# Performance work log

Measured on AMD Instinct MI355X. Metric: run time of the kernel, lower is better.

The kernel has to match this reference:

```python
import jax, jax.numpy as jnp
import numpy as np

RADIUS_IN, RADIUS_OUT, NSAMPLE = 0.4, 0.8, 32
SCENE = 10.0  # cube edge length for point coordinates


def setup_inputs() -> dict:
    key = jax.random.key(0)
    k1, k2, k3 = jax.random.split(key, 3)
    B, N, NP, C = 2, 16384, 4096, 64
    xyz = jax.random.uniform(k1, (B, N, 3), dtype=jnp.float32) * SCENE
    new_xyz = jax.random.uniform(k2, (B, NP, 3), dtype=jnp.float32) * SCENE
    features = jax.random.normal(k3, (B, C, N), dtype=jnp.float32)
    return {"xyz": xyz, "new_xyz": new_xyz, "features": features}


def ball_query_dilated(xyz, new_xyz, min_r, max_r, nsample):
    # xyz: (B,N,3), new_xyz: (B,P,3) -> idx: (B,P,nsample) int32
    N = xyz.shape[1]
    d2 = jnp.sum((new_xyz[:, :, None, :] - xyz[:, None, :, :]) ** 2, axis=-1)  # (B,P,N)
    mask = (d2 >= min_r * min_r) & (d2 < max_r * max_r)
    ar = jnp.arange(N, dtype=jnp.int32)
    # valid points keep their index; invalid pushed after all valid ones, in order
    sort_key = jnp.where(mask, ar, ar + N)
    _, idx_sorted = jax.lax.top_k(-sort_key, nsample)  # first nsample in-range point indices
    cnt = jnp.sum(mask, axis=-1)  # (B,P)
    slot_valid = jnp.arange(nsample, dtype=cnt.dtype)[None, None, :] < cnt[:, :, None]
    # CUDA kernel fills all slots with the first found index; if none found idx stays 0
    # (when cnt==0, idx_sorted[...,0] == 0 since key N is the minimum), so this matches.
    idx = jnp.where(slot_valid, idx_sorted, idx_sorted[:, :, :1])
    return idx.astype(jnp.int32)


def group(features, idx):
    # features: (B,C,N), idx: (B,P,S) -> (B,C,P,S)
    return jax.vmap(lambda f, i: f[:, i])(features, idx)


def reference(xyz, new_xyz, features):
    idx = ball_query_dilated(xyz, new_xyz, RADIUS_IN, RADIUS_OUT, NSAMPLE)
    xyz_t = jnp.transpose(xyz, (0, 2, 1))  # (B,3,N)
    grouped_xyz = group(xyz_t, idx) - jnp.transpose(new_xyz, (0, 2, 1))[:, :, :, None]
    grouped_features = group(features, idx)
    new_features = jnp.concatenate([grouped_xyz, grouped_features], axis=1)  # (B,3+C,P,S)
    return new_features
```

## Files before the change

kernel.cpp:

```cpp
#include <hip/hip_runtime.h>
#include <hip/hip_bf16.h>

#define BB 2
#define NN 16384
#define NP 4096
#define CC 64
#define SS 32
#define NCH (3 + CC)

#define NSUB 32
#define SUBN (NN / NSUB)
#define QB 32

__global__ void __launch_bounds__(256) pack_xyz_kernel(
    const float* __restrict__ xyz, float4* __restrict__ xyz4)
{
    int i = blockIdx.x * 256 + threadIdx.x;
    if (i < BB * NN) {
        float4 v;
        v.x = xyz[3 * i + 0];
        v.y = xyz[3 * i + 1];
        v.z = xyz[3 * i + 2];
        v.w = 0.0f;
        xyz4[i] = v;
    }
}

__global__ void __launch_bounds__(256) transpose_feat_kernel(
    const float* __restrict__ f, float* __restrict__ ft)
{
    __shared__ float tile[64 * 65];
    const int b  = blockIdx.y;
    const int n0 = blockIdx.x * 64;
    const int t  = threadIdx.x;
    const int tn  = t & 63;
    const int tc4 = t >> 6;
#pragma unroll
    for (int r = 0; r < 16; ++r) {
        int c = r * 4 + tc4;
        tile[c * 65 + tn] = f[((b * CC + c) << 14) + n0 + tn];
    }
    __syncthreads();
#pragma unroll
    for (int r = 0; r < 16; ++r) {
        int nl = r * 4 + tc4;
        ft[((b << 14) + n0 + nl) * CC + tn] = tile[tn * 65 + nl];
    }
}

__global__ void __launch_bounds__(256) query_kernel(
    const float4* __restrict__ xyz4, const float* __restrict__ new_xyz,
    unsigned short* __restrict__ part, unsigned char* __restrict__ cntp)
{
#pragma clang fp contract(off)
    const int lane = threadIdx.x & 63;
    const int wid  = blockIdx.x * 4 + (threadIdx.x >> 6);
    const int b    = wid >> 12;
    const int r    = wid & 4095;
    const int sub  = r >> 7;
    const int qb   = r & 127;
    const int qbase = qb * QB;

    const float RMIN2 = (float)(0.4 * 0.4);
    const float RMAX2 = (float)(0.8 * 0.8);
    const unsigned ULO  = __float_as_uint(RMIN2);
    const unsigned URNG = __float_as_uint(RMAX2) - ULO;

    const float4* __restrict__ pb = xyz4 + (b << 14) + sub * SUBN;
    float4 P[8];
#pragma unroll
    for (int k = 0; k < 8; ++k) P[k] = pb[k * 64 + lane];

    const unsigned long long ltmask = (1ull << lane) - 1ull;
    int mycnt = 0;

    for (int j = 0; j < QB; ++j) {
        const int qg = b * NP + qbase + j;
        const int qoff = __builtin_amdgcn_readfirstlane(qg * 3);
        const float qx = new_xyz[qoff + 0];
        const float qy = new_xyz[qoff + 1];
        const float qz = new_xyz[qoff + 2];

        unsigned short* __restrict__ mp = part + ((size_t)qg * NSUB + sub) * SS;
        int cnt = 0;
#pragma unroll
        for (int k = 0; k < 8; ++k) {
            float dx = P[k].x - qx;
            float dy = P[k].y - qy;
            float dz = P[k].z - qz;
            float dx2 = dx * dx;
            float dy2 = dy * dy;
            float dz2 = dz * dz;
            float d2 = (dx2 + dy2) + dz2;
            bool valid = (__float_as_uint(d2) - ULO) < URNG;
            unsigned long long m = __ballot(valid);
            if (m) {
                if (valid) {
                    int slot = cnt + (int)__popcll(m & ltmask);
                    if (slot < SS)
                        mp[slot] = (unsigned short)(sub * SUBN + k * 64 + lane);
                }
                cnt += (int)__popcll(m);
            }
        }
        if (cnt > SS) cnt = SS;
        mycnt = (lane == j) ? cnt : mycnt;
    }
    if (lane < QB)
        cntp[(size_t)(b * NP + qbase + lane) * NSUB + sub] = (unsigned char)mycnt;
}

__global__ void __launch_bounds__(256) group_kernel(
    const float4* __restrict__ xyz4, const float* __restrict__ new_xyz,
    const float* __restrict__ ft,
    const unsigned short* __restrict__ part, const unsigned char* __restrict__ cntp,
    float* __restrict__ out)
{
    __shared__ float tile[4][16 * 66];
    __shared__ int   idx_s[4][SS];
    const int w    = threadIdx.x >> 6;
    const int lane = threadIdx.x & 63;
    const int q    = blockIdx.x * 4 + w;
    const int b    = q >> 12;
    const int p    = q & (NP - 1);
    const int s    = lane & 31;

    int c = (lane < NSUB) ? (int)cntp[(size_t)q * NSUB + lane] : 0;

    int off = c;
#pragma unroll
    for (int d = 1; d < 32; d <<= 1) {
        int v = __shfl_up(off, d);
        if (lane >= d) off += v;
    }
    int total = __shfl(off, 31);
    if (total > SS) total = SS;
    off -= c;

    const unsigned short* __restrict__ pp = part + ((size_t)q * NSUB + (lane & 31)) * SS;
    int firstval = (c > 0) ? (int)pp[0] : 0;
    unsigned long long m = __ballot(c > 0);
    int first = 0;
    if (m) first = __shfl(firstval, __ffsll(m) - 1);

    for (int j = 0; j < c; ++j) {
        int sl = off + j;
        if (sl < SS) idx_s[w][sl] = (int)pp[j];
    }
    if (lane >= total && lane < SS) idx_s[w][lane] = first;
    asm volatile("s_waitcnt lgkmcnt(0)" ::: "memory");

    const int idxv = idx_s[w][s];

    float4 pt = xyz4[(b << 14) + idxv];
    float q0 = new_xyz[q * 3 + 0];
    float q1 = new_xyz[q * 3 + 1];
    float q2 = new_xyz[q * 3 + 2];
    if (lane < 32) {
        out[((b * NCH + 0) * NP + p) * SS + s] = pt.x - q0;
        out[((b * NCH + 1) * NP + p) * SS + s] = pt.y - q1;
        out[((b * NCH + 2) * NP + p) * SS + s] = pt.z - q2;
    }

    float* tl = tile[w];
    const float* __restrict__ ftb = ft + (b << 14) * CC;
    const int sl = lane & 15;
    const int cq = lane >> 4;
#pragma unroll
    for (int h = 0; h < 2; ++h) {
#pragma unroll
        for (int s2 = 0; s2 < 16; ++s2) {
            int n = __shfl(idxv, h * 16 + s2);
            tl[s2 * 66 + lane] = ftb[(n << 6) + lane];
        }
        asm volatile("s_waitcnt lgkmcnt(0)" ::: "memory");
#pragma unroll
        for (int cp = 0; cp < 16; ++cp) {
            int ch = cp * 4 + cq;
            out[((b * NCH + 3 + ch) * NP + p) * SS + h * 16 + sl] = tl[sl * 66 + ch];
        }
        asm volatile("s_waitcnt lgkmcnt(0)" ::: "memory");
    }
}

extern "C" void kernel_launch(void* const* d_in, const int* in_sizes, int n_in,
                              void* d_out, int out_size, void* d_ws, size_t ws_size,
                              hipStream_t stream)
{
    const float* xyz      = (const float*)d_in[0];
    const float* new_xyz  = (const float*)d_in[1];
    const float* features = (const float*)d_in[2];
    float* out = (float*)d_out;

    char* ws = (char*)d_ws;
    float4*         xyz4 = (float4*)(ws);
    float*          ft   = (float*)(ws + 524288);
    unsigned short* part = (unsigned short*)(ws + 8912896);
    unsigned char*  cntp = (unsigned char*)(ws + 25690112);

    hipLaunchKernelGGL(pack_xyz_kernel, dim3((BB * NN) / 256), dim3(256), 0, stream,
                       xyz, xyz4);
    hipLaunchKernelGGL(transpose_feat_kernel, dim3(NN / 64, BB), dim3(256), 0, stream,
                       features, ft);
    hipLaunchKernelGGL(query_kernel, dim3((BB * NSUB * (NP / QB)) / 4), dim3(256), 0, stream,
                       xyz4, new_xyz, part, cntp);
    hipLaunchKernelGGL(group_kernel, dim3((BB * NP) / 4), dim3(256), 0, stream,
                       xyz4, new_xyz, ft, part, cntp, out);
}
```

Baseline: 146.1 us.

## Merge feature transpose and ball query into one launch, drop xyz packing

```diff
diff --git a/kernel.cpp b/kernel.cpp
--- a/kernel.cpp
+++ b/kernel.cpp
@@ -12,49 +12,40 @@
 #define SUBN (NN / NSUB)
 #define QB 32
 
-__global__ void __launch_bounds__(256) pack_xyz_kernel(
-    const float* __restrict__ xyz, float4* __restrict__ xyz4)
-{
-    int i = blockIdx.x * 256 + threadIdx.x;
-    if (i < BB * NN) {
-        float4 v;
-        v.x = xyz[3 * i + 0];
-        v.y = xyz[3 * i + 1];
-        v.z = xyz[3 * i + 2];
-        v.w = 0.0f;
-        xyz4[i] = v;
-    }
-}
-
-__global__ void __launch_bounds__(256) transpose_feat_kernel(
-    const float* __restrict__ f, float* __restrict__ ft)
-{
-    __shared__ float tile[64 * 65];
-    const int b  = blockIdx.y;
-    const int n0 = blockIdx.x * 64;
-    const int t  = threadIdx.x;
-    const int tn  = t & 63;
-    const int tc4 = t >> 6;
-#pragma unroll
-    for (int r = 0; r < 16; ++r) {
-        int c = r * 4 + tc4;
-        tile[c * 65 + tn] = f[((b * CC + c) << 14) + n0 + tn];
-    }
-    __syncthreads();
-#pragma unroll
-    for (int r = 0; r < 16; ++r) {
-        int nl = r * 4 + tc4;
-        ft[((b << 14) + n0 + nl) * CC + tn] = tile[tn * 65 + nl];
-    }
-}
-
-__global__ void __launch_bounds__(256) query_kernel(
-    const float4* __restrict__ xyz4, const float* __restrict__ new_xyz,
+#define TBLOCKS (BB * (NN / 64))
+#define QBLOCKS ((BB * NSUB * (NP / QB)) / 4)
+
+__global__ void __launch_bounds__(256) pre_kernel(
+    const float* __restrict__ xyz, const float* __restrict__ new_xyz,
+    const float* __restrict__ f, float* __restrict__ ft,
     unsigned short* __restrict__ part, unsigned char* __restrict__ cntp)
 {
 #pragma clang fp contract(off)
+    __shared__ float tile[64 * 65];
+
+    if (blockIdx.x < TBLOCKS) {
+        const int tb = blockIdx.x;
+        const int b  = tb >> 8;
+        const int n0 = (tb & 255) << 6;
+        const int t  = threadIdx.x;
+        const int tn  = t & 63;
+        const int tc4 = t >> 6;
+#pragma unroll
+        for (int r = 0; r < 16; ++r) {
+            int c = r * 4 + tc4;
+            tile[c * 65 + tn] = f[((b * CC + c) << 14) + n0 + tn];
+        }
+        __syncthreads();
+#pragma unroll
+        for (int r = 0; r < 16; ++r) {
+            int nl = r * 4 + tc4;
+            ft[((b << 14) + n0 + nl) * CC + tn] = tile[tn * 65 + nl];
+        }
+        return;
+    }
+
     const int lane = threadIdx.x & 63;
-    const int wid  = blockIdx.x * 4 + (threadIdx.x >> 6);
+    const int wid  = (blockIdx.x - TBLOCKS) * 4 + (threadIdx.x >> 6);
     const int b    = wid >> 12;
     const int r    = wid & 4095;
     const int sub  = r >> 7;
@@ -66,10 +57,15 @@
     const unsigned ULO  = __float_as_uint(RMIN2);
     const unsigned URNG = __float_as_uint(RMAX2) - ULO;
 
-    const float4* __restrict__ pb = xyz4 + (b << 14) + sub * SUBN;
-    float4 P[8];
-#pragma unroll
-    for (int k = 0; k < 8; ++k) P[k] = pb[k * 64 + lane];
+    const int pbase = (b << 14) + sub * SUBN;
+    float px[8], py[8], pz[8];
+#pragma unroll
+    for (int k = 0; k < 8; ++k) {
+        int a3 = (pbase + k * 64 + lane) * 3;
+        px[k] = xyz[a3 + 0];
+        py[k] = xyz[a3 + 1];
+        pz[k] = xyz[a3 + 2];
+    }
 
     const unsigned long long ltmask = (1ull << lane) - 1ull;
     int mycnt = 0;
@@ -85,9 +81,9 @@
         int cnt = 0;
 #pragma unroll
         for (int k = 0; k < 8; ++k) {
-            float dx = P[k].x - qx;
-            float dy = P[k].y - qy;
-            float dz = P[k].z - qz;
+            float dx = px[k] - qx;
+            float dy = py[k] - qy;
+            float dz = pz[k] - qz;
             float dx2 = dx * dx;
             float dy2 = dy * dy;
             float dz2 = dz * dz;
@@ -111,7 +107,7 @@
 }
 
 __global__ void __launch_bounds__(256) group_kernel(
-    const float4* __restrict__ xyz4, const float* __restrict__ new_xyz,
+    const float* __restrict__ xyz, const float* __restrict__ new_xyz,
     const float* __restrict__ ft,
     const unsigned short* __restrict__ part, const unsigned char* __restrict__ cntp,
     float* __restrict__ out)
@@ -152,18 +148,21 @@
 
     const int idxv = idx_s[w][s];
 
-    float4 pt = xyz4[(b << 14) + idxv];
+    const int a3 = ((b << 14) + idxv) * 3;
+    float ptx = xyz[a3 + 0];
+    float pty = xyz[a3 + 1];
+    float ptz = xyz[a3 + 2];
     float q0 = new_xyz[q * 3 + 0];
     float q1 = new_xyz[q * 3 + 1];
     float q2 = new_xyz[q * 3 + 2];
     if (lane < 32) {
-        out[((b * NCH + 0) * NP + p) * SS + s] = pt.x - q0;
-        out[((b * NCH + 1) * NP + p) * SS + s] = pt.y - q1;
-        out[((b * NCH + 2) * NP + p) * SS + s] = pt.z - q2;
+        out[((b * NCH + 0) * NP + p) * SS + s] = ptx - q0;
+        out[((b * NCH + 1) * NP + p) * SS + s] = pty - q1;
+        out[((b * NCH + 2) * NP + p) * SS + s] = ptz - q2;
     }
 
     float* tl = tile[w];
-    const float* __restrict__ ftb = ft + (b << 14) * CC;
+    const float* __restrict__ ftb = ft + (size_t)(b << 14) * CC;
     const int sl = lane & 15;
     const int cq = lane >> 4;
 #pragma unroll
@@ -193,17 +192,12 @@
     float* out = (float*)d_out;
 
     char* ws = (char*)d_ws;
-    float4*         xyz4 = (float4*)(ws);
-    float*          ft   = (float*)(ws + 524288);
-    unsigned short* part = (unsigned short*)(ws + 8912896);
-    unsigned char*  cntp = (unsigned char*)(ws + 25690112);
-
-    hipLaunchKernelGGL(pack_xyz_kernel, dim3((BB * NN) / 256), dim3(256), 0, stream,
-                       xyz, xyz4);
-    hipLaunchKernelGGL(transpose_feat_kernel, dim3(NN / 64, BB), dim3(256), 0, stream,
-                       features, ft);
-    hipLaunchKernelGGL(query_kernel, dim3((BB * NSUB * (NP / QB)) / 4), dim3(256), 0, stream,
-                       xyz4, new_xyz, part, cntp);
+    float*          ft   = (float*)(ws);
+    unsigned short* part = (unsigned short*)(ws + 8388608);
+    unsigned char*  cntp = (unsigned char*)(ws + 25165824);
+
+    hipLaunchKernelGGL(pre_kernel, dim3(TBLOCKS + QBLOCKS), dim3(256), 0, stream,
+                       xyz, new_xyz, features, ft, part, cntp);
     hipLaunchKernelGGL(group_kernel, dim3((BB * NP) / 4), dim3(256), 0, stream,
-                       xyz4, new_xyz, ft, part, cntp, out);
+                       xyz, new_xyz, ft, part, cntp, out);
 }
```

After: 142.1 us. 1.03x faster.
